# Optimization experiments

Measured on AMD Instinct MI355X. Metric: run time of the kernel, lower is better.

## Reference

```python
import jax, jax.numpy as jnp
import numpy as np
import math

D_MODEL = 1024
N_HEADS = 16
D_K = D_MODEL // N_HEADS
B, T = 4, 2048


def setup_inputs() -> dict:
    key = jax.random.key(0)
    ks = jax.random.split(key, 5)
    s = 1.0 / math.sqrt(D_MODEL)
    return {
        "x": jax.random.normal(ks[0], (B, T, D_MODEL), dtype=jnp.float32),
        "W_qkv": jax.random.normal(ks[1], (3 * D_MODEL, D_MODEL), dtype=jnp.float32) * s,
        "b_qkv": jax.random.normal(ks[2], (3 * D_MODEL,), dtype=jnp.float32) * 0.01,
        "W_out": jax.random.normal(ks[3], (D_MODEL, D_MODEL), dtype=jnp.float32) * s,
        "b_out": jax.random.normal(ks[4], (D_MODEL,), dtype=jnp.float32) * 0.01,
    }


def reference(x, W_qkv, b_qkv, W_out, b_out):
    Bn, Tn, C = x.shape
    # qkv projection: [B,T,3C]
    qkv = jnp.einsum("btc,oc->bto", x, W_qkv) + b_qkv
    # NOTE: original reshapes to (B,T,H,3*d_k) THEN chunks -> per-head interleaved layout
    qkv = qkv.reshape(Bn, Tn, N_HEADS, 3 * D_K).transpose(0, 2, 1, 3)  # [B,H,T,3dk]
    q, k, v = jnp.split(qkv, 3, axis=-1)  # each [B,H,T,dk]
    scores = jnp.einsum("bhtd,bhsd->bhts", q, k) / math.sqrt(D_K)
    causal = jnp.tril(jnp.ones((Tn, Tn), dtype=bool))
    scores = jnp.where(causal[None, None], scores, -jnp.inf)
    attn = jax.nn.softmax(scores, axis=-1)
    ctx = jnp.einsum("bhts,bhsd->bhtd", attn, v)  # [B,H,T,dk]
    ctx = ctx.transpose(0, 2, 1, 3).reshape(Bn, Tn, C)
    return jnp.einsum("btc,oc->bto", ctx, W_out) + b_out
```

## Files before the change

kernel.cpp:

```cpp
#include <hip/hip_runtime.h>

typedef __attribute__((ext_vector_type(8))) short short8;
typedef __attribute__((ext_vector_type(4))) float f32x4;
typedef __attribute__((ext_vector_type(16))) float f32x16;
typedef __attribute__((ext_vector_type(4))) unsigned int u32x4;
typedef __attribute__((ext_vector_type(4))) unsigned short u16x4;
typedef unsigned int u32;
typedef unsigned short u16;

#define DEV static __device__ __forceinline__

DEV u16 f2bf(float f) {
  union { float f; u32 u; } c; c.f = f;
  u32 r = (c.u + 0x7fffu + ((c.u >> 16) & 1u)) >> 16;
  return (u16)r;
}
DEV float bf2f(u16 v) {
  union { u32 u; float f; } c; c.u = ((u32)v) << 16;
  return c.f;
}
DEV short8 pack8(float4 a, float4 b) {
  short8 r;
  r[0]=(short)f2bf(a.x); r[1]=(short)f2bf(a.y); r[2]=(short)f2bf(a.z); r[3]=(short)f2bf(a.w);
  r[4]=(short)f2bf(b.x); r[5]=(short)f2bf(b.y); r[6]=(short)f2bf(b.z); r[7]=(short)f2bf(b.w);
  return r;
}
DEV u32 cvtpk(float lo, float hi) {
  u32 r;
  asm("v_cvt_pk_bf16_f32 %0, %1, %2" : "=v"(r) : "v"(lo), "v"(hi));
  return r;
}

#if __has_builtin(__builtin_amdgcn_exp2f)
DEV float fexp2(float x) { return __builtin_amdgcn_exp2f(x); }
#else
DEV float fexp2(float x) { return exp2f(x); }
#endif

DEV void glds16(const void* g, void* l) {
  __builtin_amdgcn_global_load_lds((const __attribute__((address_space(1))) u32*)g,
                                   (__attribute__((address_space(3))) u32*)l, 16, 0, 0);
}

DEV f32x16 mfma32(short8 a, short8 b, f32x16 c) {
  return __builtin_amdgcn_mfma_f32_32x32x16_bf16(a, b, c, 0, 0, 0);
}

constexpr int CDIM = 1024, TT = 2048, NH = 16, DK = 64;
#define QSC 0.1803368801111601f

__global__ void conv_bf16(const float* __restrict__ X, const float* __restrict__ W1,
                          const float* __restrict__ W2, u16* __restrict__ Xb,
                          u16* __restrict__ W1b, u16* __restrict__ W2b) {
  const long n0 = 1048576, n1 = 393216, n2 = 131072;
  for (long i = (long)blockIdx.x * blockDim.x + threadIdx.x; i < n0 + n1 + n2;
       i += (long)gridDim.x * blockDim.x) {
    const float* s; u16* d; long j = i;
    if (j < n0) { s = X; d = Xb; }
    else if (j < n0 + n1) { j -= n0; s = W1; d = W1b; }
    else { j -= n0 + n1; s = W2; d = W2b; }
    float4 a = ((const float4*)s)[2 * j];
    float4 b = ((const float4*)s)[2 * j + 1];
    ((short8*)d)[j] = pack8(a, b);
  }
}

__global__ void qkv_gemm2(const u16* __restrict__ A, const u16* __restrict__ B,
                          const float* __restrict__ bias, u16* __restrict__ Qb,
                          u16* __restrict__ Kb, u16* __restrict__ VTb) {
  __shared__ u16 As[128][64];
  __shared__ u16 Bs[128][64];
  const int tid = threadIdx.x, lane = tid & 63, wv = tid >> 6;
  const int wr = wv >> 1, wc = wv & 1, lo = lane & 15, lg = lane >> 4;
  const int m0 = blockIdx.x * 128, n0 = blockIdx.y * 128;
  const int rin = lane >> 3, blk = lane & 7;

  f32x4 acc[4][4];
  const f32x4 fz = {0.f, 0.f, 0.f, 0.f};
#pragma unroll
  for (int i = 0; i < 4; ++i)
#pragma unroll
    for (int j = 0; j < 4; ++j) acc[i][j] = fz;

  for (int k0 = 0; k0 < CDIM; k0 += 64) {
    const u16* ga = A + (size_t)(m0 + 32 * wv + rin) * CDIM + k0 + blk * 8;
    const u16* gb = B + (size_t)(n0 + 32 * wv + rin) * CDIM + k0 + blk * 8;
#pragma unroll
    for (int i = 0; i < 4; ++i) glds16(ga + (size_t)(8 * i) * CDIM, &As[32 * wv + 8 * i][0]);
#pragma unroll
    for (int i = 0; i < 4; ++i) glds16(gb + (size_t)(8 * i) * CDIM, &Bs[32 * wv + 8 * i][0]);
    __syncthreads();
#pragma unroll
    for (int kk = 0; kk < 2; ++kk) {
      short8 af[4], bf[4];
#pragma unroll
      for (int mi = 0; mi < 4; ++mi) af[mi] = *(const short8*)&As[wr * 64 + mi * 16 + lo][kk * 32 + lg * 8];
#pragma unroll
      for (int ni = 0; ni < 4; ++ni) bf[ni] = *(const short8*)&Bs[wc * 64 + ni * 16 + lo][kk * 32 + lg * 8];
#pragma unroll
      for (int mi = 0; mi < 4; ++mi)
#pragma unroll
        for (int ni = 0; ni < 4; ++ni)
          acc[mi][ni] = __builtin_amdgcn_mfma_f32_16x16x32_bf16(af[mi], bf[ni], acc[mi][ni], 0, 0, 0);
    }
    __syncthreads();
  }

#pragma unroll
  for (int ni = 0; ni < 4; ++ni) {
    const int o = n0 + wc * 64 + ni * 16 + lo;
    const float bv = bias[o];
    const int h = o / 192, rem = o - h * 192, which = rem >> 6, d = rem & 63;
#pragma unroll
    for (int mi = 0; mi < 4; ++mi) {
      const int mb = m0 + wr * 64 + mi * 16 + lg * 4;
      const int bb = mb >> 11, t0 = mb & 2047;
      const int bh = bb * NH + h;
      if (which == 2) {
        u16x4 pk;
#pragma unroll
        for (int r = 0; r < 4; ++r) pk[r] = f2bf(acc[mi][ni][r] + bv);
        *(u16x4*)&VTb[((size_t)bh * DK + d) * TT + t0] = pk;
      } else if (which == 1) {
#pragma unroll
        for (int r = 0; r < 4; ++r)
          Kb[((size_t)bh * TT + t0 + r) * DK + d] = f2bf(acc[mi][ni][r] + bv);
      } else {
#pragma unroll
        for (int r = 0; r < 4; ++r)
          Qb[((size_t)bh * TT + t0 + r) * DK + d] = f2bf((acc[mi][ni][r] + bv) * QSC);
      }
    }
  }
}

__global__ void __launch_bounds__(256, 4)
attn10(const u16* __restrict__ Qb, const u16* __restrict__ Kb,
       const u16* __restrict__ VTb, u16* __restrict__ PA, u16* __restrict__ PB,
       float* __restrict__ ML) {
  __shared__ u16 Kls[2][64][64];
  __shared__ u16 Vls[2][64][64];
  const int tid = threadIdx.x, lane = tid & 63, wv = tid >> 6;
  const int lq = lane & 31, h = lane >> 5;
  const int id = blockIdx.x;
  const int w = (id & 7) * 128 + (id >> 3);
  const int bh = w >> 4;
  const int pj = w & 7;
  const int sp = (w >> 3) & 1;
  const int bb = bh >> 4, head = bh & 15;
  const u16* Qp = Qb + (size_t)bh * TT * DK;
  const u16* Kp = Kb + (size_t)bh * TT * DK;
  const u16* Vp = VTb + (size_t)bh * DK * TT;
  const int rin = lane >> 3, blk = lane & 7;
  u16* PO = sp ? PB : PA;

  const u16* kga = Kp + (size_t)(wv * 16 + rin) * DK + (blk ^ rin) * 8;
  const u16* vga = Vp + (size_t)(wv * 16 + rin) * TT + (blk ^ rin) * 8;
  u16* kls0 = &Kls[0][wv * 16][0];
  u16* vls0 = &Vls[0][wv * 16][0];
  const int lds_half = 64 * 64;

#define STAGE10(bufi, kvt_)                                                 \
  {                                                                         \
    const int o_ = (bufi) * lds_half;                                       \
    glds16(kga + (size_t)(kvt_) * 4096, kls0 + o_);                         \
    glds16(kga + (size_t)(kvt_) * 4096 + 512, kls0 + o_ + 512);             \
    glds16(vga + (size_t)(kvt_) * 64, vls0 + o_);                           \
    glds16(vga + (size_t)(kvt_) * 64 + 8 * TT, vls0 + o_ + 512);            \
  }

  for (int pi = 0; pi < 2; ++pi) {
    const int qtile = pi ? (15 - pj) : pj;
    const int q0w = qtile * 128 + wv * 32;
    const int qrow = q0w + lq;

    short8 qw[4];
#pragma unroll
    for (int kk = 0; kk < 4; ++kk)
      qw[kk] = *(const short8*)&Qp[(size_t)qrow * DK + kk * 16 + h * 8];

    f32x16 oa0, oa1;
#pragma unroll
    for (int r = 0; r < 16; ++r) { oa0[r] = 0.f; oa1[r] = 0.f; }
    float l_s = 0.f;

    const int nt = 2 * qtile + 2;
    STAGE10(0, sp);
    __syncthreads();
    int buf = 0;
    for (int kvt = sp; kvt < nt; kvt += 2) {
      const int kv0 = kvt * 64;
      if (kvt + 2 < nt) STAGE10(buf ^ 1, kvt + 2);
      if (kv0 <= q0w + 31) {
        f32x16 s0, s1;
#pragma unroll
        for (int r = 0; r < 16; ++r) { s0[r] = 0.f; s1[r] = 0.f; }
        __builtin_amdgcn_s_setprio(1);
#pragma unroll
        for (int kk = 0; kk < 4; ++kk) {
          const short8 kf0 = *(const short8*)&Kls[buf][lq][(((2 * kk + h) ^ (lq & 7)) * 8)];
          const short8 kf1 = *(const short8*)&Kls[buf][32 + lq][(((2 * kk + h) ^ (lq & 7)) * 8)];
          s0 = mfma32(kf0, qw[kk], s0);
          s1 = mfma32(kf1, qw[kk], s1);
        }
        __builtin_amdgcn_s_setprio(0);
        const bool diag = (kv0 + 63 > q0w);
        if (diag) {
          const int lim = qrow - kv0 - 4 * h;
#pragma unroll
          for (int r = 0; r < 16; ++r) {
            const int kl = (r & 3) + 8 * (r >> 2);
            s0[r] = (kl <= lim) ? s0[r] : -1e30f;
            s1[r] = (kl + 32 <= lim) ? s1[r] : -1e30f;
          }
        }
        float rsa = 0.f, rsb = 0.f, rsc = 0.f, rsd = 0.f;
#pragma unroll
        for (int r = 0; r < 16; r += 4) {
          const float a0 = fexp2(s0[r]),     a1 = fexp2(s1[r]);
          const float b0 = fexp2(s0[r + 1]), b1 = fexp2(s1[r + 1]);
          const float c0 = fexp2(s0[r + 2]), c1 = fexp2(s1[r + 2]);
          const float d0 = fexp2(s0[r + 3]), d1 = fexp2(s1[r + 3]);
          s0[r] = a0; s1[r] = a1; s0[r + 1] = b0; s1[r + 1] = b1;
          s0[r + 2] = c0; s1[r + 2] = c1; s0[r + 3] = d0; s1[r + 3] = d1;
          rsa += a0 + a1; rsb += b0 + b1; rsc += c0 + c1; rsd += d0 + d1;
        }
        float rs = (rsa + rsb) + (rsc + rsd);
        rs += __shfl_xor(rs, 32);
        l_s += rs;
#pragma unroll
        for (int s = 0; s < 2; ++s) {
          u32 C[8];
#pragma unroll
          for (int j = 0; j < 8; ++j)
            C[j] = s ? cvtpk(s1[2 * j], s1[2 * j + 1]) : cvtpk(s0[2 * j], s0[2 * j + 1]);
#pragma unroll
          for (int b = 0; b < 2; ++b) {
            const int o = 4 * b;
            const u32 D1 = h ? C[o + 0] : C[o + 2];
            const u32 D2 = h ? C[o + 1] : C[o + 3];
            const u32 R1 = __shfl_xor(D1, 32);
            const u32 R2 = __shfl_xor(D2, 32);
            union { u32x4 w; short8 s8; } pa;
            pa.w[0] = h ? R1 : C[o + 0];
            pa.w[1] = h ? R2 : C[o + 1];
            pa.w[2] = h ? C[o + 2] : R1;
            pa.w[3] = h ? C[o + 3] : R2;
            const int ks = 2 * s + b;
            const short8 vb0 = *(const short8*)&Vls[buf][lq][(((2 * ks + h) ^ (lq & 7)) * 8)];
            const short8 vb1 = *(const short8*)&Vls[buf][32 + lq][(((2 * ks + h) ^ (lq & 7)) * 8)];
            __builtin_amdgcn_s_setprio(1);
            oa0 = mfma32(pa.s8, vb0, oa0);
            oa1 = mfma32(pa.s8, vb1, oa1);
            __builtin_amdgcn_s_setprio(0);
          }
        }
      }
      __syncthreads();
      buf ^= 1;
    }

#pragma unroll
    for (int r = 0; r < 16; ++r) {
      const int t = q0w + (r & 3) + 8 * (r >> 2) + 4 * h;
      const size_t rowb = ((size_t)(bb * TT + t)) * CDIM + head * DK;
      PO[rowb + lq] = f2bf(oa0[r]);
      PO[rowb + 32 + lq] = f2bf(oa1[r]);
    }
    if (h == 0) ML[((size_t)(sp * 64 + bh) << 11) + qrow] = l_s;
    __syncthreads();
  }
#undef STAGE10
}

__global__ void attn_merge(const u16* PA, const u16* PB,
                           const float* __restrict__ ML, u16* Ctx) {
  const int row = blockIdx.x;
  const int b = row >> 11, t = row & 2047;
  const int c = threadIdx.x * 4;
  const int head = c >> 6;
  const int bh = b * NH + head;
  const float lA = ML[((size_t)bh << 11) + t];
  const float lB = ML[((size_t)(64 + bh) << 11) + t];
  const float il = 1.0f / (lA + lB);
  const size_t idx = ((size_t)row) * CDIM + c;
  u16x4 pa = *(const u16x4*)&PA[idx];
  u16x4 pb = *(const u16x4*)&PB[idx];
  u16x4 o;
#pragma unroll
  for (int e = 0; e < 4; ++e) o[e] = f2bf((bf2f(pa[e]) + bf2f(pb[e])) * il);
  *(u16x4*)&Ctx[idx] = o;
}

__global__ void out_gemm2(const u16* __restrict__ A, const u16* __restrict__ B,
                          const float* __restrict__ bias, float* __restrict__ Out) {
  __shared__ u16 As[128][64];
  __shared__ u16 Bs[128][64];
  const int tid = threadIdx.x, lane = tid & 63, wv = tid >> 6;
  const int wr = wv >> 1, wc = wv & 1, lo = lane & 15, lg = lane >> 4;
  const int m0 = blockIdx.x * 128, n0 = blockIdx.y * 128;
  const int rin = lane >> 3, blk = lane & 7;

  f32x4 acc[4][4];
  const f32x4 fz = {0.f, 0.f, 0.f, 0.f};
#pragma unroll
  for (int i = 0; i < 4; ++i)
#pragma unroll
    for (int j = 0; j < 4; ++j) acc[i][j] = fz;

  for (int k0 = 0; k0 < CDIM; k0 += 64) {
    const u16* ga = A + (size_t)(m0 + 32 * wv + rin) * CDIM + k0 + blk * 8;
    const u16* gb = B + (size_t)(n0 + 32 * wv + rin) * CDIM + k0 + blk * 8;
#pragma unroll
    for (int i = 0; i < 4; ++i) glds16(ga + (size_t)(8 * i) * CDIM, &As[32 * wv + 8 * i][0]);
#pragma unroll
    for (int i = 0; i < 4; ++i) glds16(gb + (size_t)(8 * i) * CDIM, &Bs[32 * wv + 8 * i][0]);
    __syncthreads();
#pragma unroll
    for (int kk = 0; kk < 2; ++kk) {
      short8 af[4], bf[4];
#pragma unroll
      for (int mi = 0; mi < 4; ++mi) af[mi] = *(const short8*)&As[wr * 64 + mi * 16 + lo][kk * 32 + lg * 8];
#pragma unroll
      for (int ni = 0; ni < 4; ++ni) bf[ni] = *(const short8*)&Bs[wc * 64 + ni * 16 + lo][kk * 32 + lg * 8];
#pragma unroll
      for (int mi = 0; mi < 4; ++mi)
#pragma unroll
        for (int ni = 0; ni < 4; ++ni)
          acc[mi][ni] = __builtin_amdgcn_mfma_f32_16x16x32_bf16(af[mi], bf[ni], acc[mi][ni], 0, 0, 0);
    }
    __syncthreads();
  }

#pragma unroll
  for (int ni = 0; ni < 4; ++ni) {
    const int o = n0 + wc * 64 + ni * 16 + lo;
    const float bv = bias[o];
#pragma unroll
    for (int mi = 0; mi < 4; ++mi)
#pragma unroll
      for (int r = 0; r < 4; ++r)
        Out[(size_t)(m0 + wr * 64 + mi * 16 + lg * 4 + r) * CDIM + o] = acc[mi][ni][r] + bv;
  }
}

extern "C" void kernel_launch(void* const* d_in, const int* in_sizes, int n_in,
                              void* d_out, int out_size, void* d_ws, size_t ws_size,
                              hipStream_t stream) {
  const float* X = (const float*)d_in[0];
  const float* Wqkv = (const float*)d_in[1];
  const float* bqkv = (const float*)d_in[2];
  const float* Wout = (const float*)d_in[3];
  const float* bout = (const float*)d_in[4];
  float* Out = (float*)d_out;

  u16* Xb  = (u16*)d_ws;
  u16* W1b = Xb + 8388608;
  u16* W2b = W1b + 3145728;
  u16* Qb  = W2b + 1048576;
  u16* Kb  = Qb + 8388608;
  u16* VTb = Kb + 8388608;
  u16* Ctx = VTb + 8388608;

  conv_bf16<<<1024, 256, 0, stream>>>(X, Wqkv, Wout, Xb, W1b, W2b);
  qkv_gemm2<<<dim3(64, 24), 256, 0, stream>>>(Xb, W1b, bqkv, Qb, Kb, VTb);
  attn10<<<dim3(1024), 256, 0, stream>>>(Qb, Kb, VTb, Ctx, Xb, (float*)W1b);
  attn_merge<<<8192, 256, 0, stream>>>(Ctx, Xb, (const float*)W1b, Ctx);
  out_gemm2<<<dim3(64, 8), 256, 0, stream>>>(Ctx, W2b, bout, Out);
}
```

Measured before the change: 165.7 us.

## Rewrite QKV GEMM with triple-buffered async LDS pipeline and swizzled tiles

Replaces the QKV projection GEMM with a 256x128 tile, 512-thread kernel. Global-to-LDS loads are triple-buffered and controlled by explicit vmcnt waits, so loads for later k-steps overlap MFMA work. The LDS layout is XOR-swizzled to avoid bank conflicts, and block IDs are remapped so neighbouring blocks share tiles in L2. This adds a large 147KB LDS footprint and hand-tuned wait counts, which limits occupancy and makes correctness depend on the count of outstanding loads.

Measured after the change: 180.7 us. 1.09x slower.

```diff
diff --git a/kernel.cpp b/kernel.cpp
--- a/kernel.cpp
+++ b/kernel.cpp
@@ -65,15 +65,35 @@
   }
 }
 
-__global__ void qkv_gemm2(const u16* __restrict__ A, const u16* __restrict__ B,
-                          const float* __restrict__ bias, u16* __restrict__ Qb,
-                          u16* __restrict__ Kb, u16* __restrict__ VTb) {
-  __shared__ u16 As[128][64];
-  __shared__ u16 Bs[128][64];
-  const int tid = threadIdx.x, lane = tid & 63, wv = tid >> 6;
-  const int wr = wv >> 1, wc = wv & 1, lo = lane & 15, lg = lane >> 4;
-  const int m0 = blockIdx.x * 128, n0 = blockIdx.y * 128;
+__global__ void __launch_bounds__(512, 2)
+qkv_gemm3(const u16* __restrict__ A, const u16* __restrict__ B,
+          const float* __restrict__ bias, u16* __restrict__ Qb,
+          u16* __restrict__ Kb, u16* __restrict__ VTb) {
+  __shared__ u16 LS[3][3][128][64];
+  const int tid = threadIdx.x, lane = tid & 63, wid = tid >> 6;
+  const int lo = lane & 15, lg = lane >> 4;
+  const int wm = wid >> 1, wn = wid & 1;
   const int rin = lane >> 3, blk = lane & 7;
+  const int id = blockIdx.x;
+  const int w = (id & 7) * 96 + (id >> 3);
+  const int m0 = (w & 31) * 256, n0 = (w >> 5) * 128;
+  const int r7 = lo & 7;
+
+  const u16* gA = A + (size_t)(m0 + wid * 16 + rin) * CDIM + (blk ^ rin) * 8;
+  const u16* gB = B + (size_t)(n0 + wid * 16 + rin) * CDIM + (blk ^ rin) * 8;
+  u16* lsb = &LS[0][0][wid * 16][0];
+
+#define STG3(bufi, kt)                                           \
+  {                                                              \
+    const int k0e = (kt) * 64;                                   \
+    u16* lb = lsb + (bufi) * 24576;                              \
+    glds16(gA + k0e, lb);                                        \
+    glds16(gA + k0e + 8 * CDIM, lb + 512);                       \
+    glds16(gA + k0e + 128 * CDIM, lb + 8192);                    \
+    glds16(gA + k0e + 136 * CDIM, lb + 8704);                    \
+    glds16(gB + k0e, lb + 16384);                                \
+    glds16(gB + k0e + 8 * CDIM, lb + 16896);                     \
+  }
 
   f32x4 acc[4][4];
   const f32x4 fz = {0.f, 0.f, 0.f, 0.f};
@@ -82,40 +102,58 @@
 #pragma unroll
     for (int j = 0; j < 4; ++j) acc[i][j] = fz;
 
-  for (int k0 = 0; k0 < CDIM; k0 += 64) {
-    const u16* ga = A + (size_t)(m0 + 32 * wv + rin) * CDIM + k0 + blk * 8;
-    const u16* gb = B + (size_t)(n0 + 32 * wv + rin) * CDIM + k0 + blk * 8;
-#pragma unroll
-    for (int i = 0; i < 4; ++i) glds16(ga + (size_t)(8 * i) * CDIM, &As[32 * wv + 8 * i][0]);
-#pragma unroll
-    for (int i = 0; i < 4; ++i) glds16(gb + (size_t)(8 * i) * CDIM, &Bs[32 * wv + 8 * i][0]);
-    __syncthreads();
-#pragma unroll
-    for (int kk = 0; kk < 2; ++kk) {
-      short8 af[4], bf[4];
-#pragma unroll
-      for (int mi = 0; mi < 4; ++mi) af[mi] = *(const short8*)&As[wr * 64 + mi * 16 + lo][kk * 32 + lg * 8];
-#pragma unroll
-      for (int ni = 0; ni < 4; ++ni) bf[ni] = *(const short8*)&Bs[wc * 64 + ni * 16 + lo][kk * 32 + lg * 8];
+  STG3(0, 0);
+  STG3(1, 1);
+  int b0 = 0, b1 = 1, b2 = 2;
+  for (int T = 0; T < 16; ++T) {
+    if (T < 14) {
+      STG3(b2, T + 2);
+      asm volatile("s_waitcnt vmcnt(12)" ::: "memory");
+    } else if (T == 14) {
+      asm volatile("s_waitcnt vmcnt(6)" ::: "memory");
+    } else {
+      asm volatile("s_waitcnt vmcnt(0)" ::: "memory");
+    }
+    __builtin_amdgcn_s_barrier();
+    {
+      const u16* pA = &LS[b0][wm >> 1][(wm & 1) * 64][0];
+      const u16* pB = &LS[b0][2][wn * 64][0];
+      short8 af[4][2], bfr[4][2];
 #pragma unroll
       for (int mi = 0; mi < 4; ++mi)
 #pragma unroll
-        for (int ni = 0; ni < 4; ++ni)
-          acc[mi][ni] = __builtin_amdgcn_mfma_f32_16x16x32_bf16(af[mi], bf[ni], acc[mi][ni], 0, 0, 0);
-    }
-    __syncthreads();
-  }
+        for (int kk = 0; kk < 2; ++kk)
+          af[mi][kk] = *(const short8*)&pA[(mi * 16 + lo) * 64 + (((kk * 4 + lg) ^ r7) * 8)];
+#pragma unroll
+      for (int ni = 0; ni < 4; ++ni)
+#pragma unroll
+        for (int kk = 0; kk < 2; ++kk)
+          bfr[ni][kk] = *(const short8*)&pB[(ni * 16 + lo) * 64 + (((kk * 4 + lg) ^ r7) * 8)];
+      __builtin_amdgcn_s_setprio(1);
+#pragma unroll
+      for (int kk = 0; kk < 2; ++kk)
+#pragma unroll
+        for (int mi = 0; mi < 4; ++mi)
+#pragma unroll
+          for (int ni = 0; ni < 4; ++ni)
+            acc[mi][ni] = __builtin_amdgcn_mfma_f32_16x16x32_bf16(af[mi][kk], bfr[ni][kk], acc[mi][ni], 0, 0, 0);
+      __builtin_amdgcn_s_setprio(0);
+    }
+    __builtin_amdgcn_s_barrier();
+    const int tmp = b0; b0 = b1; b1 = b2; b2 = tmp;
+  }
+#undef STG3
 
 #pragma unroll
   for (int ni = 0; ni < 4; ++ni) {
-    const int o = n0 + wc * 64 + ni * 16 + lo;
+    const int o = n0 + wn * 64 + ni * 16 + lo;
     const float bv = bias[o];
-    const int h = o / 192, rem = o - h * 192, which = rem >> 6, d = rem & 63;
+    const int hh = o / 192, rem = o - hh * 192, which = rem >> 6, d = rem & 63;
 #pragma unroll
     for (int mi = 0; mi < 4; ++mi) {
-      const int mb = m0 + wr * 64 + mi * 16 + lg * 4;
-      const int bb = mb >> 11, t0 = mb & 2047;
-      const int bh = bb * NH + h;
+      const int mb = m0 + wm * 64 + mi * 16 + lg * 4;
+      const int bbi = mb >> 11, t0 = mb & 2047;
+      const int bh = bbi * NH + hh;
       if (which == 2) {
         u16x4 pk;
 #pragma unroll
@@ -363,7 +401,7 @@
   u16* Ctx = VTb + 8388608;
 
   conv_bf16<<<1024, 256, 0, stream>>>(X, Wqkv, Wout, Xb, W1b, W2b);
-  qkv_gemm2<<<dim3(64, 24), 256, 0, stream>>>(Xb, W1b, bqkv, Qb, Kb, VTb);
+  qkv_gemm3<<<dim3(768), 512, 0, stream>>>(Xb, W1b, bqkv, Qb, Kb, VTb);
   attn10<<<dim3(1024), 256, 0, stream>>>(Qb, Kb, VTb, Ctx, Xb, (float*)W1b);
   attn_merge<<<8192, 256, 0, stream>>>(Ctx, Xb, (const float*)W1b, Ctx);
   out_gemm2<<<dim3(64, 8), 256, 0, stream>>>(Ctx, W2b, bout, Out);
```
